# Optimization experiments

Measured on AMD Instinct MI355X. Metric: run time of the kernel, lower is better.

## Reference

```python
import jax, jax.numpy as jnp
import numpy as np


def setup_inputs() -> dict:
    key = jax.random.key(0)
    ks = jax.random.split(key, 10)
    B, D_X, D_H, D_S, D_T = 16384, 256, 512, 128, 128
    G = 4 * D_H
    sc = lambda d: 1.0 / np.sqrt(d)
    return {
        "x": jax.random.normal(ks[0], (B, D_X), jnp.float32),
        "h": jax.random.normal(ks[1], (B, D_H), jnp.float32),
        "c": jax.random.normal(ks[2], (B, D_H), jnp.float32),
        "spatial_per_step": jax.random.normal(ks[3], (B, D_S), jnp.float32),
        "temporal_per_step": jax.random.normal(ks[4], (B, D_T), jnp.float32),
        "W_x": jax.random.normal(ks[5], (D_X, G), jnp.float32) * sc(D_X),
        "W_h": jax.random.normal(ks[6], (D_H, G), jnp.float32) * sc(D_H),
        "b_h": jax.random.normal(ks[7], (G,), jnp.float32) * 0.01,
        "W_s": jax.random.normal(ks[8], (D_S, G), jnp.float32) * sc(D_S),
        "W_t": jax.random.normal(ks[9], (D_T, G), jnp.float32) * sc(D_T),
    }


def reference(x, h, c, spatial_per_step, temporal_per_step, W_x, W_h, b_h, W_s, W_t):
    H = W_h.shape[0]  # hidden_size
    # Four gate projections summed (the fusion opportunity): [B, 4H]
    preact = (x @ W_x) + (h @ W_h + b_h) + (spatial_per_step @ W_s) + (temporal_per_step @ W_t)
    i_g = jax.nn.sigmoid(preact[:, 0 * H:1 * H])
    f_g = jax.nn.sigmoid(preact[:, 1 * H:2 * H])
    o_g = jax.nn.sigmoid(preact[:, 2 * H:3 * H])
    c_g = jnp.tanh(preact[:, 3 * H:4 * H])
    c_new = f_g * c + i_g * c_g
    # NOTE: faithful to the source, h = tanh(o * c) (not o * tanh(c))
    h_new = jnp.tanh(o_g * c_new)
    return (h_new, c_new)
```

## Files before the change

kernel.cpp:

```cpp
#include <hip/hip_runtime.h>
#include <hip/hip_bf16.h>
#include <cstdint>

#define B_DIM 16384
#define DX 256
#define DH 512
#define DS 128
#define DT 128
#define KDIM 1024
#define NDIM 2048
#define HOUT 512

typedef __attribute__((ext_vector_type(8))) short short8;
typedef __attribute__((ext_vector_type(4))) float floatx4;

union bf16x8 {
  short8 v;
  __hip_bfloat16 b[8];
};

__device__ __forceinline__ float fast_sigmoid(float x) {
  return 1.f / (1.f + __expf(-x));
}
__device__ __forceinline__ float fast_tanh(float x) {
  float e = __expf(-2.f * x);
  return (1.f - e) / (1.f + e);
}


__global__ __launch_bounds__(256) void pack_A(
    const float* __restrict__ x, const float* __restrict__ h,
    const float* __restrict__ s, const float* __restrict__ t,
    __hip_bfloat16* __restrict__ Ap) {
  int tid = blockIdx.x * 256 + threadIdx.x;
  int r = tid >> 7;
  int k = (tid & 127) * 8;
  const float* p;
  if (k < 768) {
    p = (k < 256) ? (x + (size_t)r * DX + k) : (h + (size_t)r * DH + (k - 256));
  } else {
    p = (k < 896) ? (s + (size_t)r * DS + (k - 768)) : (t + (size_t)r * DT + (k - 896));
  }
  floatx4 v0 = *(const floatx4*)p;
  floatx4 v1 = *(const floatx4*)(p + 4);
  bf16x8 o;
#pragma unroll
  for (int j = 0; j < 4; ++j) {
    o.b[j]     = __float2bfloat16(v0[j]);
    o.b[4 + j] = __float2bfloat16(v1[j]);
  }
  *(short8*)(Ap + (size_t)tid * 8) = o.v;
}

__global__ __launch_bounds__(256) void pack_W(
    const float* __restrict__ Wx, const float* __restrict__ Wh,
    const float* __restrict__ Ws, const float* __restrict__ Wt,
    __hip_bfloat16* __restrict__ Wp) {
  int tid = blockIdx.x * 256 + threadIdx.x;
  int i = tid & 63;
  int tt = (tid >> 6) & 15;
  int tile = tid >> 10;
  int kb = tile & 15, nblk = tile >> 4;
  int sp = tt >> 3, c = tt & 7;
  int nl = c * 16 + (i >> 2);
  int k = kb * 64 + sp * 32 + (i & 3) * 8;
  int wn = nl >> 6, g = (nl >> 4) & 3, hl = nl & 15;
  int col = g * 512 + nblk * 32 + wn * 16 + hl;
  const float* src; int kl;
  if (k < 256)      { src = Wx; kl = k; }
  else if (k < 768) { src = Wh; kl = k - 256; }
  else if (k < 896) { src = Ws; kl = k - 768; }
  else              { src = Wt; kl = k - 896; }
  bf16x8 o;
#pragma unroll
  for (int r = 0; r < 8; ++r)
    o.b[r] = __float2bfloat16(src[(size_t)(kl + r) * NDIM + col]);
  *(short8*)(Wp + (size_t)tid * 8) = o.v;
}

__global__ __launch_bounds__(256, 4) void lstm_gemm(
    const __hip_bfloat16* __restrict__ Ap, const __hip_bfloat16* __restrict__ Wp,
    const float* __restrict__ bh, const float* __restrict__ c_in,
    float* __restrict__ out) {
  __shared__ unsigned short As[128 * 32];
  __shared__ unsigned short Bs[128 * 32];

  const int tid = threadIdx.x;
  const int lane = tid & 63;
  const int wid = tid >> 6;
  const int wm = wid & 1;
  const int wn = wid >> 1;
  const int q = lane >> 4;
  const int fr = lane & 15;
  const int mb = blockIdx.y;
  const int nblk = blockIdx.x;
  const int m0 = mb * 128;

  floatx4 acc[4][4];
#pragma unroll
  for (int i = 0; i < 4; ++i)
#pragma unroll
    for (int j = 0; j < 4; ++j) acc[i][j] = (floatx4)0.f;

  const int arow_in_chunk = lane >> 2;
  const int akoff = (lane & 3) * 8;

  for (int p = 0; p < 32; ++p) {
    const int k0 = p * 32;
    const size_t bbase = ((size_t)((nblk * 16 + (p >> 1)) * 16 + (p & 1) * 8)) * 512;
#pragma unroll
    for (int j = 0; j < 2; ++j) {
      const int chunk = wid * 2 + j;
      __builtin_amdgcn_global_load_lds(
          (const __attribute__((address_space(1))) void*)
              (Ap + (size_t)(m0 + chunk * 16 + arow_in_chunk) * KDIM + k0 + akoff),
          (__attribute__((address_space(3))) void*)&As[chunk * 512], 16, 0, 0);
      __builtin_amdgcn_global_load_lds(
          (const __attribute__((address_space(1))) void*)
              (Wp + bbase + (size_t)chunk * 512 + lane * 8),
          (__attribute__((address_space(3))) void*)&Bs[chunk * 512], 16, 0, 0);
    }
    __syncthreads();

    short8 af[4], bf[4];
#pragma unroll
    for (int i = 0; i < 4; ++i) {
      af[i] = *(const short8*)&As[(wm * 64 + i * 16 + fr) * 32 + q * 8];
      bf[i] = *(const short8*)&Bs[(wn * 64 + i * 16 + fr) * 32 + q * 8];
    }
#pragma unroll
    for (int mi = 0; mi < 4; ++mi)
#pragma unroll
      for (int ni = 0; ni < 4; ++ni)
        acc[mi][ni] = __builtin_amdgcn_mfma_f32_16x16x32_bf16(
            af[mi], bf[ni], acc[mi][ni], 0, 0, 0);
    __syncthreads();
  }

  const int hh = nblk * 32 + wn * 16 + fr;
  float bias[4];
#pragma unroll
  for (int g = 0; g < 4; ++g) bias[g] = bh[g * 512 + hh];

#pragma unroll
  for (int mi = 0; mi < 4; ++mi) {
#pragma unroll
    for (int r = 0; r < 4; ++r) {
      const size_t grow = (size_t)(m0 + wm * 64 + mi * 16 + q * 4 + r);
      const float pi = acc[mi][0][r] + bias[0];
      const float pf = acc[mi][1][r] + bias[1];
      const float po = acc[mi][2][r] + bias[2];
      const float pc = acc[mi][3][r] + bias[3];
      const float ig = fast_sigmoid(pi);
      const float fg = fast_sigmoid(pf);
      const float og = fast_sigmoid(po);
      const float cg = fast_tanh(pc);
      const float cc = fg * c_in[grow * HOUT + hh] + ig * cg;
      out[grow * HOUT + hh] = fast_tanh(og * cc);
      out[(size_t)B_DIM * HOUT + grow * HOUT + hh] = cc;
    }
  }
}

extern "C" void kernel_launch(void* const* d_in, const int* in_sizes, int n_in,
                              void* d_out, int out_size, void* d_ws, size_t ws_size,
                              hipStream_t stream) {
  const float* x  = (const float*)d_in[0];
  const float* h  = (const float*)d_in[1];
  const float* c  = (const float*)d_in[2];
  const float* sp = (const float*)d_in[3];
  const float* tp = (const float*)d_in[4];
  const float* Wx = (const float*)d_in[5];
  const float* Wh = (const float*)d_in[6];
  const float* bh = (const float*)d_in[7];
  const float* Ws = (const float*)d_in[8];
  const float* Wt = (const float*)d_in[9];
  float* out = (float*)d_out;

  __hip_bfloat16* Ap = (__hip_bfloat16*)d_ws;
  __hip_bfloat16* Wp = (__hip_bfloat16*)((char*)d_ws + (size_t)B_DIM * KDIM * 2);

  pack_A<<<dim3(B_DIM * KDIM / 8 / 256), dim3(256), 0, stream>>>(x, h, sp, tp, Ap);
  pack_W<<<dim3(NDIM * KDIM / 8 / 256), dim3(256), 0, stream>>>(Wx, Wh, Ws, Wt, Wp);
  lstm_gemm<<<dim3(NDIM / 128, B_DIM / 128), dim3(256), 0, stream>>>(Ap, Wp, bh, c, out);
}
```

Measured before the change: 241.9 us.

## Rewrite LSTM GEMM with 256x256 tiles and a triple-buffered LDS pipeline

The GEMM moves to 512-thread blocks that each compute a 256x256 output tile, with a three-slot LDS ring filled by global_load_lds so loads run two k-steps ahead of the MFMAs. LDS reads use an XOR swizzle to avoid bank conflicts, and the block order is remapped for L2 locality. pack_W is rewritten to emit a plain column-major K-contiguous layout that matches the new tile loads. The goal is to hide memory latency and raise arithmetic intensity. The cost is higher register pressure (32 accumulators per thread) and a 96KB dynamic LDS footprint that limits occupancy.

```diff
diff --git a/kernel.cpp b/kernel.cpp
--- a/kernel.cpp
+++ b/kernel.cpp
@@ -10,6 +10,9 @@
 #define KDIM 1024
 #define NDIM 2048
 #define HOUT 512
+
+#define NT 32
+#define SLOT 8192
 
 typedef __attribute__((ext_vector_type(8))) short short8;
 typedef __attribute__((ext_vector_type(4))) float floatx4;
@@ -57,20 +60,16 @@
     const float* __restrict__ Ws, const float* __restrict__ Wt,
     __hip_bfloat16* __restrict__ Wp) {
   int tid = blockIdx.x * 256 + threadIdx.x;
-  int i = tid & 63;
-  int tt = (tid >> 6) & 15;
-  int tile = tid >> 10;
-  int kb = tile & 15, nblk = tile >> 4;
-  int sp = tt >> 3, c = tt & 7;
-  int nl = c * 16 + (i >> 2);
-  int k = kb * 64 + sp * 32 + (i & 3) * 8;
-  int wn = nl >> 6, g = (nl >> 4) & 3, hl = nl & 15;
-  int col = g * 512 + nblk * 32 + wn * 16 + hl;
+  int pcol = tid >> 7;
+  int k0 = (tid & 127) * 8;
+  int nb = pcol >> 8, rr = pcol & 255;
+  int wn = rr >> 6, g = (rr >> 4) & 3, hl = rr & 15;
+  int col = g * 512 + nb * 64 + wn * 16 + hl;
   const float* src; int kl;
-  if (k < 256)      { src = Wx; kl = k; }
-  else if (k < 768) { src = Wh; kl = k - 256; }
-  else if (k < 896) { src = Ws; kl = k - 768; }
-  else              { src = Wt; kl = k - 896; }
+  if (k0 < 256)      { src = Wx; kl = k0; }
+  else if (k0 < 768) { src = Wh; kl = k0 - 256; }
+  else if (k0 < 896) { src = Ws; kl = k0 - 768; }
+  else               { src = Wt; kl = k0 - 896; }
   bf16x8 o;
 #pragma unroll
   for (int r = 0; r < 8; ++r)
@@ -78,12 +77,18 @@
   *(short8*)(Wp + (size_t)tid * 8) = o.v;
 }
 
-__global__ __launch_bounds__(256, 4) void lstm_gemm(
+#define GLD(src, dst)                                              \
+  __builtin_amdgcn_global_load_lds(                                \
+      (const __attribute__((address_space(1))) void*)(src),        \
+      (__attribute__((address_space(3))) void*)(dst), 16, 0, 0)
+
+__global__ __launch_bounds__(512, 2) void lstm_gemm(
     const __hip_bfloat16* __restrict__ Ap, const __hip_bfloat16* __restrict__ Wp,
     const float* __restrict__ bh, const float* __restrict__ c_in,
     float* __restrict__ out) {
-  __shared__ unsigned short As[128 * 32];
-  __shared__ unsigned short Bs[128 * 32];
+  extern __shared__ unsigned short smem[];
+  unsigned short* As = smem;
+  unsigned short* Bs = smem + 3 * SLOT;
 
   const int tid = threadIdx.x;
   const int lane = tid & 63;
@@ -92,61 +97,109 @@
   const int wn = wid >> 1;
   const int q = lane >> 4;
   const int fr = lane & 15;
-  const int mb = blockIdx.y;
-  const int nblk = blockIdx.x;
-  const int m0 = mb * 128;
-
-  floatx4 acc[4][4];
-#pragma unroll
-  for (int i = 0; i < 4; ++i)
+
+  const int bid = blockIdx.x;
+  const int wg = (bid & 7) * 64 + (bid >> 3);
+  const int mb = wg >> 3;
+  const int nb = wg & 7;
+  const int m0 = mb * 256;
+
+  int aOff[8], bOff[4];
+#pragma unroll
+  for (int m = 0; m < 8; ++m) {
+    int row = wm * 128 + m * 16 + fr;
+    aOff[m] = row * 32 + (q ^ ((row >> 1) & 3)) * 8;
+  }
+#pragma unroll
+  for (int n = 0; n < 4; ++n) {
+    int colc = wn * 64 + n * 16 + fr;
+    bOff[n] = colc * 32 + (q ^ ((colc >> 1) & 3)) * 8;
+  }
+
+  const int srow = wid * 16 + (lane >> 2);
+  const int qlin = lane & 3;
+  const int q0 = qlin ^ ((srow >> 1) & 3);
+  const int srow1 = srow + 128;
+  const int q1 = qlin ^ ((srow1 >> 1) & 3);
+  const __hip_bfloat16* aS0 = Ap + (size_t)(m0 + srow)  * KDIM + q0 * 8;
+  const __hip_bfloat16* aS1 = Ap + (size_t)(m0 + srow1) * KDIM + q1 * 8;
+  const __hip_bfloat16* bS0 = Wp + (size_t)(nb * 256 + srow)  * KDIM + q0 * 8;
+  const __hip_bfloat16* bS1 = Wp + (size_t)(nb * 256 + srow1) * KDIM + q1 * 8;
+
+  const int dH0 = wid * 512;
+  const int dH1 = 4096 + wid * 512;
+
+  floatx4 acc[8][4];
+#pragma unroll
+  for (int i = 0; i < 8; ++i)
 #pragma unroll
     for (int j = 0; j < 4; ++j) acc[i][j] = (floatx4)0.f;
 
-  const int arow_in_chunk = lane >> 2;
-  const int akoff = (lane & 3) * 8;
-
-  for (int p = 0; p < 32; ++p) {
-    const int k0 = p * 32;
-    const size_t bbase = ((size_t)((nblk * 16 + (p >> 1)) * 16 + (p & 1) * 8)) * 512;
-#pragma unroll
-    for (int j = 0; j < 2; ++j) {
-      const int chunk = wid * 2 + j;
-      __builtin_amdgcn_global_load_lds(
-          (const __attribute__((address_space(1))) void*)
-              (Ap + (size_t)(m0 + chunk * 16 + arow_in_chunk) * KDIM + k0 + akoff),
-          (__attribute__((address_space(3))) void*)&As[chunk * 512], 16, 0, 0);
-      __builtin_amdgcn_global_load_lds(
-          (const __attribute__((address_space(1))) void*)
-              (Wp + bbase + (size_t)chunk * 512 + lane * 8),
-          (__attribute__((address_space(3))) void*)&Bs[chunk * 512], 16, 0, 0);
-    }
-    __syncthreads();
-
-    short8 af[4], bf[4];
-#pragma unroll
-    for (int i = 0; i < 4; ++i) {
-      af[i] = *(const short8*)&As[(wm * 64 + i * 16 + fr) * 32 + q * 8];
-      bf[i] = *(const short8*)&Bs[(wn * 64 + i * 16 + fr) * 32 + q * 8];
-    }
-#pragma unroll
-    for (int mi = 0; mi < 4; ++mi)
-#pragma unroll
-      for (int ni = 0; ni < 4; ++ni)
-        acc[mi][ni] = __builtin_amdgcn_mfma_f32_16x16x32_bf16(
-            af[mi], bf[ni], acc[mi][ni], 0, 0, 0);
-    __syncthreads();
-  }
-
-  const int hh = nblk * 32 + wn * 16 + fr;
+  GLD(aS0,      &As[dH0]);        GLD(aS1,      &As[dH1]);
+  GLD(bS0,      &Bs[dH0]);        GLD(bS1,      &Bs[dH1]);
+  GLD(aS0 + 32, &As[SLOT + dH0]); GLD(aS1 + 32, &As[SLOT + dH1]);
+  GLD(bS0 + 32, &Bs[SLOT + dH0]); GLD(bS1 + 32, &Bs[SLOT + dH1]);
+  asm volatile("s_waitcnt vmcnt(4)\n\ts_barrier" ::: "memory");
+
+  int sR = 0;
+  int sS = 2 * SLOT;
+
+  for (int t = 0; t < NT; ++t) {
+    const int ts = (t < NT - 2) ? (t + 2) : (NT - 1);
+    const int kO = ts * 32;
+    const unsigned short* Ar = As + sR;
+    const unsigned short* Br = Bs + sR;
+
+    short8 a0[4], bv[4];
+#pragma unroll
+    for (int m = 0; m < 4; ++m) a0[m] = *(const short8*)(Ar + aOff[m]);
+#pragma unroll
+    for (int n = 0; n < 4; ++n) bv[n] = *(const short8*)(Br + bOff[n]);
+    GLD(aS0 + kO, &As[sS + dH0]);
+    GLD(aS1 + kO, &As[sS + dH1]);
+    asm volatile("s_barrier" ::: "memory");
+    __builtin_amdgcn_sched_barrier(0);
+    __builtin_amdgcn_s_setprio(1);
+#pragma unroll
+    for (int m = 0; m < 4; ++m)
+#pragma unroll
+      for (int n = 0; n < 4; ++n)
+        acc[m][n] = __builtin_amdgcn_mfma_f32_16x16x32_bf16(a0[m], bv[n],
+                                                            acc[m][n], 0, 0, 0);
+    __builtin_amdgcn_s_setprio(0);
+    asm volatile("s_barrier" ::: "memory");
+
+    short8 a1[4];
+#pragma unroll
+    for (int m = 0; m < 4; ++m) a1[m] = *(const short8*)(Ar + aOff[4 + m]);
+    GLD(bS0 + kO, &Bs[sS + dH0]);
+    GLD(bS1 + kO, &Bs[sS + dH1]);
+    asm volatile("s_barrier" ::: "memory");
+    __builtin_amdgcn_sched_barrier(0);
+    __builtin_amdgcn_s_setprio(1);
+#pragma unroll
+    for (int m = 0; m < 4; ++m)
+#pragma unroll
+      for (int n = 0; n < 4; ++n)
+        acc[4 + m][n] = __builtin_amdgcn_mfma_f32_16x16x32_bf16(a1[m], bv[n],
+                                                                acc[4 + m][n], 0, 0, 0);
+    __builtin_amdgcn_s_setprio(0);
+    asm volatile("s_waitcnt vmcnt(4)\n\ts_barrier" ::: "memory");
+
+    sR = (sR == 2 * SLOT) ? 0 : sR + SLOT;
+    sS = (sS == 2 * SLOT) ? 0 : sS + SLOT;
+  }
+
+  const int hh = nb * 64 + wn * 16 + fr;
   float bias[4];
 #pragma unroll
   for (int g = 0; g < 4; ++g) bias[g] = bh[g * 512 + hh];
 
 #pragma unroll
-  for (int mi = 0; mi < 4; ++mi) {
+  for (int mi = 0; mi < 8; ++mi) {
 #pragma unroll
     for (int r = 0; r < 4; ++r) {
-      const size_t grow = (size_t)(m0 + wm * 64 + mi * 16 + q * 4 + r);
+      const size_t grow = (size_t)(m0 + wm * 128 + mi * 16 + q * 4 + r);
       const float pi = acc[mi][0][r] + bias[0];
       const float pf = acc[mi][1][r] + bias[1];
       const float po = acc[mi][2][r] + bias[2];
@@ -180,7 +233,14 @@
   __hip_bfloat16* Ap = (__hip_bfloat16*)d_ws;
   __hip_bfloat16* Wp = (__hip_bfloat16*)((char*)d_ws + (size_t)B_DIM * KDIM * 2);
 
+  static bool attr_done = false;
+  if (!attr_done) {
+    hipFuncSetAttribute((const void*)lstm_gemm,
+                        hipFuncAttributeMaxDynamicSharedMemorySize, 98304);
+    attr_done = true;
+  }
+
   pack_A<<<dim3(B_DIM * KDIM / 8 / 256), dim3(256), 0, stream>>>(x, h, sp, tp, Ap);
   pack_W<<<dim3(NDIM * KDIM / 8 / 256), dim3(256), 0, stream>>>(Wx, Wh, Ws, Wt, Wp);
-  lstm_gemm<<<dim3(NDIM / 128, B_DIM / 128), dim3(256), 0, stream>>>(Ap, Wp, bh, c, out);
-}
+  lstm_gemm<<<dim3(512), dim3(512), 98304, stream>>>(Ap, Wp, bh, c, out);
+}
```

Result: slower. 254.5 us (+5.2%).
